# Kernel tuning notes

Measured on AMD Instinct MI355X. Metric: run time of the kernel, lower is better.

Reference implementation:

```python
import jax, jax.numpy as jnp
import numpy as np

B, P, D_IN = 128, 4096, 4   # frames, points/frame, xyz+time
NG = 16                      # number of trajectory groups
H1, H2, H3 = 64, 128, 512    # PointNet shared-MLP widths


def _init_mlp(key, dims):
    ks = jax.random.split(key, len(dims) - 1)
    params = []
    for k, (di, do) in zip(ks, zip(dims[:-1], dims[1:])):
        W = jax.random.normal(k, (di, do), dtype=jnp.float32) * (1.0 / np.sqrt(di))
        b = jnp.zeros((do,), dtype=jnp.float32)
        params.append((W, b))
    return params


def setup_inputs() -> dict:
    key = jax.random.key(0)
    k_pc, k_t, k_idx, k_g, k_l = jax.random.split(key, 5)
    pc = jax.random.normal(k_pc, (B, 3, P), dtype=jnp.float32)
    traj_time_batch = jax.random.uniform(k_t, (B, 1), dtype=jnp.float32)
    traj_inbatch_index = jnp.sort(jax.random.randint(k_idx, (B,), 0, NG)).astype(jnp.int32)
    (Wg1, bg1), (Wg2, bg2), (Wg3, bg3) = _init_mlp(k_g, [D_IN, H1, H2, H3])
    (Wl1, bl1), (Wl2, bl2), (Wl3, bl3) = _init_mlp(k_l, [D_IN, H1, H2, H3])
    return dict(pc=pc, traj_time_batch=traj_time_batch, traj_inbatch_index=traj_inbatch_index,
                Wg1=Wg1, bg1=bg1, Wg2=Wg2, bg2=bg2, Wg3=Wg3, bg3=bg3,
                Wl1=Wl1, bl1=bl1, Wl2=Wl2, bl2=bl2, Wl3=Wl3, bl3=bl3)


def _mlp(x, layers):
    # pointwise shared MLP: x [..., P, d_in] -> [..., P, d_out]
    for W, b in layers:
        x = jax.nn.relu(x @ W + b)
    return x


def reference(pc, traj_time_batch, traj_inbatch_index,
              Wg1, bg1, Wg2, bg2, Wg3, bg3,
              Wl1, bl1, Wl2, bl2, Wl3, bl3):
    b, _, p = pc.shape
    # append time channel: [B,3,P] + [B,1,P] -> [B,4,P]
    t = jnp.broadcast_to(traj_time_batch[..., None], (b, 1, p))
    feat = jnp.concatenate([pc, t], axis=1)
    x = jnp.swapaxes(feat, 1, 2)  # [B,P,4] points-last layout for pointwise MLP

    # global branch: shared MLP on every point, then max over all points of each trajectory group
    hg = _mlp(x, [(Wg1, bg1), (Wg2, bg2), (Wg3, bg3)])           # [B,P,H3]
    seg = jnp.repeat(traj_inbatch_index, p)                       # [B*P]
    gmax = jax.ops.segment_max(hg.reshape(b * p, -1), seg, num_segments=NG)  # [NG,H3]
    global_feat = gmax[traj_inbatch_index]                        # [B,H3] broadcast back per frame

    # local branch: per-frame PointNet encode (shared MLP + max over points)
    hl = _mlp(x, [(Wl1, bl1), (Wl2, bl2), (Wl3, bl3)])            # [B,P,H3]
    local_feat = hl.max(axis=1)                                   # [B,H3]

    z = jnp.concatenate([global_feat, local_feat], axis=1)        # [B,2*H3]
    input_features_vis = pc                                       # original pc (last dim == 4096, no slice)
    return (z, input_features_vis)
```

## Files before the change

kernel.cpp:

```cpp
#include <hip/hip_runtime.h>
#include <hip/hip_bf16.h>

#define NB   128
#define NP   4096
#define NGRP 16
#define C3   512

typedef __bf16 bf16x8 __attribute__((ext_vector_type(8)));
typedef __bf16 bf16x4 __attribute__((ext_vector_type(4)));
typedef float  f32x4  __attribute__((ext_vector_type(4)));

#define WS_W1F_G 0
#define WS_W1F_L 4096
#define WS_W2F_G 8192
#define WS_W2F_L 24576
#define WS_W3F_G 40960
#define WS_W3F_L 172032
#define WS_GMAX  303104

__global__ __launch_bounds__(256) void prep_kernel(
    const float* __restrict__ Wg1, const float* __restrict__ Wg2, const float* __restrict__ Wg3,
    const float* __restrict__ Wl1, const float* __restrict__ Wl2, const float* __restrict__ Wl3,
    const float* __restrict__ pc, float* __restrict__ out, char* __restrict__ ws) {
    const int t = blockIdx.x, tid = threadIdx.x;
    if (t >= 37) {
        const f32x4* src = (const f32x4*)pc;
        f32x4* dst = (f32x4*)(out + NB * 2 * C3);
        int base = (t - 37) * 1024 + tid;
        #pragma unroll
        for (int j = 0; j < 4; ++j) dst[base + j * 256] = src[base + j * 256];
        return;
    }
    if (t == 36) {
        float* gmax = (float*)(ws + WS_GMAX);
        #pragma unroll
        for (int k = 0; k < 32; ++k) gmax[k * 256 + tid] = 0.0f;
        int c = tid >> 6, lane = tid & 63;
        int ch = c * 16 + (lane & 15);
        int kb = (lane >> 4) * 8;
        bf16x8 pg, pl;
        #pragma unroll
        for (int j = 0; j < 8; ++j) {
            int k = kb + j;
            pg[j] = (k < 4) ? (__bf16)Wg1[k * 64 + ch] : (__bf16)0.0f;
            pl[j] = (k < 4) ? (__bf16)Wl1[k * 64 + ch] : (__bf16)0.0f;
        }
        *(bf16x8*)((__bf16*)(ws + WS_W1F_G) + c * 512 + lane * 8) = pg;
        *(bf16x8*)((__bf16*)(ws + WS_W1F_L) + c * 512 + lane * 8) = pl;
        return;
    }
    __shared__ float tile[64][65];
    const float* src; __bf16* dst; int cBase, mMul, srcStride;
    if (t < 32) {
        int branch = t >> 4, rem = t & 15;
        int tk = rem >> 3, tc = rem & 7;
        src = (branch ? Wl3 : Wg3) + (size_t)(tk * 64) * 512 + tc * 64;
        dst = (__bf16*)(ws + (branch ? WS_W3F_L : WS_W3F_G));
        cBase = tc * 16 + tk * 2; mMul = 4; srcStride = 512;
    } else {
        int u = t - 32; int branch = u >> 1, tc = u & 1;
        src = (branch ? Wl2 : Wg2) + tc * 64;
        dst = (__bf16*)(ws + (branch ? WS_W2F_L : WS_W2F_G));
        cBase = tc * 8; mMul = 2; srcStride = 128;
    }
    {
        int r0 = tid >> 6, cl = tid & 63;
        #pragma unroll
        for (int p = 0; p < 16; ++p)
            tile[p * 4 + r0][cl] = src[(size_t)(p * 4 + r0) * srcStride + cl];
    }
    __syncthreads();
    int lane = tid & 63, l15 = lane & 15, q = lane >> 4;
    #pragma unroll
    for (int cc = 0; cc < 2; ++cc) {
        int pair = (tid >> 6) * 2 + cc;
        int mi = pair >> 1, ks = pair & 1;
        bf16x8 pk;
        #pragma unroll
        for (int j = 0; j < 8; ++j) pk[j] = (__bf16)tile[ks * 32 + q * 8 + j][mi * 16 + l15];
        *(bf16x8*)(dst + (cBase + mi * mMul + ks) * 512 + lane * 8) = pk;
    }
}

__global__ __launch_bounds__(512, 2) void main_kernel(
    const float* __restrict__ pc, const float* __restrict__ tt, const int* __restrict__ idx,
    const float* __restrict__ bg1, const float* __restrict__ bg2, const float* __restrict__ bg3,
    const float* __restrict__ bl1, const float* __restrict__ bl2, const float* __restrict__ bl3,
    float* __restrict__ out, char* __restrict__ ws) {
    __shared__ __align__(16) char smem[102912];
    __bf16* h2f = (__bf16*)smem;
    __bf16* w2f = (__bf16*)(smem + 65536);
    __bf16* h1s = (__bf16*)(smem + 81920);
    float*  b2s = (float*)(smem + 102400);

    const int tid = threadIdx.x, lane = tid & 63, wave = tid >> 6;
    const int quad = lane >> 4, l15 = lane & 15;
    const int branch = blockIdx.y, frame = blockIdx.x;

    const __bf16* w1g = (const __bf16*)(ws + (branch ? WS_W1F_L : WS_W1F_G));
    const __bf16* w2g = (const __bf16*)(ws + (branch ? WS_W2F_L : WS_W2F_G));
    const __bf16* w3g = (const __bf16*)(ws + (branch ? WS_W3F_L : WS_W3F_G));
    const float* b1 = branch ? bl1 : bg1;
    const float* b2 = branch ? bl2 : bg2;
    const float* b3 = branch ? bl3 : bg3;

    for (int i = tid; i < 1024; i += 512) ((f32x4*)w2f)[i] = ((const f32x4*)w2g)[i];
    if (tid < 128) b2s[tid] = b2[tid];

    bf16x8 a1[4];
    #pragma unroll
    for (int mi = 0; mi < 4; ++mi) a1[mi] = *(const bf16x8*)(w1g + mi * 512 + lane * 8);
    bf16x8 aw[4][4];
    #pragma unroll
    for (int mi = 0; mi < 4; ++mi)
        #pragma unroll
        for (int ks = 0; ks < 4; ++ks)
            aw[mi][ks] = *(const bf16x8*)(w3g + (wave * 16 + mi * 4 + ks) * 512 + lane * 8);

    float b1r[4][4];
    #pragma unroll
    for (int mi = 0; mi < 4; ++mi)
        #pragma unroll
        for (int r = 0; r < 4; ++r) b1r[mi][r] = b1[mi * 16 + quad * 4 + r];

    const float tval = tt[frame];
    const f32x4 zf = {0.0f, 0.0f, 0.0f, 0.0f};
    f32x4 runmax[4];
    #pragma unroll
    for (int mi = 0; mi < 4; ++mi) runmax[mi] = (f32x4){-1e30f, -1e30f, -1e30f, -1e30f};

    const float* pcx = pc + (size_t)frame * 3 * NP;
    __bf16* hs = h1s + wave * 1280;
    const int pw = wave * 16 + l15;

    float xx = pcx[pw], xy = pcx[NP + pw], xz = pcx[2 * NP + pw];

    __syncthreads();

    {
        bf16x8 xb;
        #pragma unroll
        for (int j = 0; j < 8; ++j) xb[j] = (__bf16)0.0f;
        if (quad == 0) { xb[0] = (__bf16)xx; xb[1] = (__bf16)xy; xb[2] = (__bf16)xz; xb[3] = (__bf16)tval; }
        #pragma unroll
        for (int mi = 0; mi < 4; ++mi) {
            f32x4 c = __builtin_amdgcn_mfma_f32_16x16x32_bf16(a1[mi], xb, zf, 0, 0, 0);
            bf16x4 pk;
            #pragma unroll
            for (int r = 0; r < 4; ++r) pk[r] = (__bf16)fmaxf(c[r] + b1r[mi][r], 0.0f);
            *(bf16x4*)(hs + l15 * 80 + mi * 16 + quad * 4) = pk;
        }
        bf16x8 hbf0 = *(const bf16x8*)(hs + l15 * 80 + quad * 8);
        bf16x8 hbf1 = *(const bf16x8*)(hs + l15 * 80 + 32 + quad * 8);
        #pragma unroll
        for (int mi = 0; mi < 8; ++mi) {
            bf16x8 a20 = *(const bf16x8*)(w2f + (mi * 2) * 512 + lane * 8);
            bf16x8 a21 = *(const bf16x8*)(w2f + (mi * 2 + 1) * 512 + lane * 8);
            f32x4 c = __builtin_amdgcn_mfma_f32_16x16x32_bf16(a20, hbf0, zf, 0, 0, 0);
            c = __builtin_amdgcn_mfma_f32_16x16x32_bf16(a21, hbf1, c, 0, 0, 0);
            f32x4 bb = *(const f32x4*)(b2s + mi * 16 + quad * 4);
            bf16x4 pk;
            #pragma unroll
            for (int r = 0; r < 4; ++r) pk[r] = (__bf16)fmaxf(c[r] + bb[r], 0.0f);
            const int c0 = mi * 16 + quad * 4;
            *(bf16x4*)(h2f + ((wave * 4 + (c0 >> 5)) * 4 + ((c0 >> 3) & 3)) * 128 + l15 * 8 + (c0 & 7)) = pk;
        }
    }

    for (int m = 0; m < 32; ++m) {
        __syncthreads();
        const __bf16* hb = h2f + (m & 1) * 16384;
        __bf16* hbn = h2f + ((m + 1) & 1) * 16384;
        const bool more = (m < 31);
        float nx = 0.f, ny = 0.f, nz = 0.f;
        if (more) {
            const int p = (m + 1) * 128 + pw;
            nx = pcx[p]; ny = pcx[NP + p]; nz = pcx[2 * NP + p];
        }
        bf16x8 hbf0, hbf1;
        bf16x8 bh0[4], bh1[4];
        #pragma unroll
        for (int ks = 0; ks < 4; ++ks) bh0[ks] = *(const bf16x8*)(hb + ks * 512 + lane * 8);
        #pragma unroll
        for (int ni = 0; ni < 8; ++ni) {
            bf16x8* cur = (ni & 1) ? bh1 : bh0;
            bf16x8* nxt = (ni & 1) ? bh0 : bh1;
            if (ni < 7) {
                #pragma unroll
                for (int ks = 0; ks < 4; ++ks)
                    nxt[ks] = *(const bf16x8*)(hb + ((ni + 1) * 4 + ks) * 512 + lane * 8);
            }
            f32x4 acc[4];
            #pragma unroll
            for (int ks = 0; ks < 4; ++ks)
                #pragma unroll
                for (int mi = 0; mi < 4; ++mi)
                    acc[mi] = __builtin_amdgcn_mfma_f32_16x16x32_bf16(
                        aw[mi][ks], cur[ks], ks ? acc[mi] : zf, 0, 0, 0);
            #pragma unroll
            for (int mi = 0; mi < 4; ++mi)
                #pragma unroll
                for (int r = 0; r < 4; ++r)
                    runmax[mi][r] = fmaxf(runmax[mi][r], acc[mi][r]);

            if (more && ni == 2) {
                bf16x8 xb;
                #pragma unroll
                for (int j = 0; j < 8; ++j) xb[j] = (__bf16)0.0f;
                if (quad == 0) { xb[0] = (__bf16)nx; xb[1] = (__bf16)ny; xb[2] = (__bf16)nz; xb[3] = (__bf16)tval; }
                #pragma unroll
                for (int mi = 0; mi < 4; ++mi) {
                    f32x4 c = __builtin_amdgcn_mfma_f32_16x16x32_bf16(a1[mi], xb, zf, 0, 0, 0);
                    bf16x4 pk;
                    #pragma unroll
                    for (int r = 0; r < 4; ++r) pk[r] = (__bf16)fmaxf(c[r] + b1r[mi][r], 0.0f);
                    *(bf16x4*)(hs + l15 * 80 + mi * 16 + quad * 4) = pk;
                }
            }
            if (more && ni == 4) {
                hbf0 = *(const bf16x8*)(hs + l15 * 80 + quad * 8);
                hbf1 = *(const bf16x8*)(hs + l15 * 80 + 32 + quad * 8);
            }
            if (more && ni == 6) {
                #pragma unroll
                for (int mi = 0; mi < 8; ++mi) {
                    bf16x8 a20 = *(const bf16x8*)(w2f + (mi * 2) * 512 + lane * 8);
                    bf16x8 a21 = *(const bf16x8*)(w2f + (mi * 2 + 1) * 512 + lane * 8);
                    f32x4 c = __builtin_amdgcn_mfma_f32_16x16x32_bf16(a20, hbf0, zf, 0, 0, 0);
                    c = __builtin_amdgcn_mfma_f32_16x16x32_bf16(a21, hbf1, c, 0, 0, 0);
                    f32x4 bb = *(const f32x4*)(b2s + mi * 16 + quad * 4);
                    bf16x4 pk;
                    #pragma unroll
                    for (int r = 0; r < 4; ++r) pk[r] = (__bf16)fmaxf(c[r] + bb[r], 0.0f);
                    const int c0 = mi * 16 + quad * 4;
                    *(bf16x4*)(hbn + ((wave * 4 + (c0 >> 5)) * 4 + ((c0 >> 3) & 3)) * 128 + l15 * 8 + (c0 & 7)) = pk;
                }
            }
        }
    }

    const int g = idx[frame];
    float* gmax = (float*)(ws + WS_GMAX);
    #pragma unroll
    for (int mi = 0; mi < 4; ++mi) {
        f32x4 v = runmax[mi];
        #pragma unroll
        for (int d = 1; d < 16; d <<= 1) {
            #pragma unroll
            for (int r = 0; r < 4; ++r) v[r] = fmaxf(v[r], __shfl_xor(v[r], d));
        }
        if (l15 == 0) {
            #pragma unroll
            for (int r = 0; r < 4; ++r) {
                const int ch = wave * 64 + mi * 16 + quad * 4 + r;
                const float fv = fmaxf(v[r] + b3[ch], 0.0f);
                if (branch == 0)
                    atomicMax((unsigned*)(gmax + g * C3 + ch), __float_as_uint(fv));
                else
                    out[(size_t)frame * (2 * C3) + C3 + ch] = fv;
            }
        }
    }
}

__global__ void gather_kernel(const int* __restrict__ idx, const char* __restrict__ ws,
                              float* __restrict__ out) {
    int i = blockIdx.x * blockDim.x + threadIdx.x;
    int b = i >> 9, ch = i & 511;
    const float* gmax = (const float*)(ws + WS_GMAX);
    out[b * (2 * C3) + ch] = gmax[idx[b] * C3 + ch];
}

extern "C" void kernel_launch(void* const* d_in, const int* in_sizes, int n_in,
                              void* d_out, int out_size, void* d_ws, size_t ws_size,
                              hipStream_t stream) {
    const float* pc  = (const float*)d_in[0];
    const float* tt  = (const float*)d_in[1];
    const int*   idx = (const int*)d_in[2];
    const float* Wg1 = (const float*)d_in[3];  const float* bg1 = (const float*)d_in[4];
    const float* Wg2 = (const float*)d_in[5];  const float* bg2 = (const float*)d_in[6];
    const float* Wg3 = (const float*)d_in[7];  const float* bg3 = (const float*)d_in[8];
    const float* Wl1 = (const float*)d_in[9];  const float* bl1 = (const float*)d_in[10];
    const float* Wl2 = (const float*)d_in[11]; const float* bl2 = (const float*)d_in[12];
    const float* Wl3 = (const float*)d_in[13]; const float* bl3 = (const float*)d_in[14];
    float* out = (float*)d_out;
    char*  ws  = (char*)d_ws;

    prep_kernel<<<421, 256, 0, stream>>>(Wg1, Wg2, Wg3, Wl1, Wl2, Wl3, pc, out, ws);
    main_kernel<<<dim3(128, 2), 512, 0, stream>>>(pc, tt, idx, bg1, bg2, bg3,
                                                  bl1, bl2, bl3, out, ws);
    gather_kernel<<<256, 256, 0, stream>>>(idx, ws, out);
}
```

Measured before the change: 202.2 us.

## Split layer-3 channels across wave slices and compute layer-2 cooperatively per block

Reorganizes main_kernel so each wave holds a 128-channel slice of W3 (8x4 fragments) covering half the points, and layers 1 and 2 are computed cooperatively with W2 fragments held in registers instead of LDS. Per-wave maxima are combined through shared memory before the bias, ReLU and atomic or store. The pc passthrough copy moves from prep_kernel into main_kernel's branch-0 blocks, shrinking the prep launch. This trades more register pressure (32 W3 fragments per wave) and extra barriers for better operand reuse and less LDS traffic and footprint.

```diff
diff --git a/kernel.cpp b/kernel.cpp
--- a/kernel.cpp
+++ b/kernel.cpp
@@ -21,16 +21,8 @@
 __global__ __launch_bounds__(256) void prep_kernel(
     const float* __restrict__ Wg1, const float* __restrict__ Wg2, const float* __restrict__ Wg3,
     const float* __restrict__ Wl1, const float* __restrict__ Wl2, const float* __restrict__ Wl3,
-    const float* __restrict__ pc, float* __restrict__ out, char* __restrict__ ws) {
+    char* __restrict__ ws) {
     const int t = blockIdx.x, tid = threadIdx.x;
-    if (t >= 37) {
-        const f32x4* src = (const f32x4*)pc;
-        f32x4* dst = (f32x4*)(out + NB * 2 * C3);
-        int base = (t - 37) * 1024 + tid;
-        #pragma unroll
-        for (int j = 0; j < 4; ++j) dst[base + j * 256] = src[base + j * 256];
-        return;
-    }
     if (t == 36) {
         float* gmax = (float*)(ws + WS_GMAX);
         #pragma unroll
@@ -87,15 +79,24 @@
     const float* __restrict__ bg1, const float* __restrict__ bg2, const float* __restrict__ bg3,
     const float* __restrict__ bl1, const float* __restrict__ bl2, const float* __restrict__ bl3,
     float* __restrict__ out, char* __restrict__ ws) {
-    __shared__ __align__(16) char smem[102912];
+    __shared__ __align__(16) char smem[82688];
     __bf16* h2f = (__bf16*)smem;
-    __bf16* w2f = (__bf16*)(smem + 65536);
-    __bf16* h1s = (__bf16*)(smem + 81920);
-    float*  b2s = (float*)(smem + 102400);
+    __bf16* h1f = (__bf16*)(smem + 65536);
+    float*  b1s = (float*)(smem + 81920);
+    float*  b2s = (float*)(smem + 82176);
 
     const int tid = threadIdx.x, lane = tid & 63, wave = tid >> 6;
     const int quad = lane >> 4, l15 = lane & 15;
     const int branch = blockIdx.y, frame = blockIdx.x;
+    const int half = wave >> 2;
+    const int slice = wave & 3;
+
+    if (branch == 0) {
+        const f32x4* ps = (const f32x4*)(pc + (size_t)frame * 3 * NP);
+        f32x4* pd = (f32x4*)(out + NB * 2 * C3 + (size_t)frame * 3 * NP);
+        #pragma unroll
+        for (int j = 0; j < 6; ++j) pd[j * 512 + tid] = ps[j * 512 + tid];
+    }
 
     const __bf16* w1g = (const __bf16*)(ws + (branch ? WS_W1F_L : WS_W1F_G));
     const __bf16* w2g = (const __bf16*)(ws + (branch ? WS_W2F_L : WS_W2F_G));
@@ -104,40 +105,35 @@
     const float* b2 = branch ? bl2 : bg2;
     const float* b3 = branch ? bl3 : bg3;
 
-    for (int i = tid; i < 1024; i += 512) ((f32x4*)w2f)[i] = ((const f32x4*)w2g)[i];
+    if (tid < 64)  b1s[tid] = b1[tid];
     if (tid < 128) b2s[tid] = b2[tid];
 
     bf16x8 a1[4];
     #pragma unroll
     for (int mi = 0; mi < 4; ++mi) a1[mi] = *(const bf16x8*)(w1g + mi * 512 + lane * 8);
-    bf16x8 aw[4][4];
-    #pragma unroll
-    for (int mi = 0; mi < 4; ++mi)
+    bf16x8 a2[2][2];
+    #pragma unroll
+    for (int mi = 0; mi < 2; ++mi)
+        #pragma unroll
+        for (int ks = 0; ks < 2; ++ks)
+            a2[mi][ks] = *(const bf16x8*)(w2g + ((slice * 2 + mi) * 2 + ks) * 512 + lane * 8);
+    bf16x8 aw[8][4];
+    #pragma unroll
+    for (int mi = 0; mi < 8; ++mi)
         #pragma unroll
         for (int ks = 0; ks < 4; ++ks)
-            aw[mi][ks] = *(const bf16x8*)(w3g + (wave * 16 + mi * 4 + ks) * 512 + lane * 8);
-
-    float b1r[4][4];
-    #pragma unroll
-    for (int mi = 0; mi < 4; ++mi)
-        #pragma unroll
-        for (int r = 0; r < 4; ++r) b1r[mi][r] = b1[mi * 16 + quad * 4 + r];
+            aw[mi][ks] = *(const bf16x8*)(w3g + ((slice * 8 + mi) * 4 + ks) * 512 + lane * 8);
 
     const float tval = tt[frame];
     const f32x4 zf = {0.0f, 0.0f, 0.0f, 0.0f};
-    f32x4 runmax[4];
-    #pragma unroll
-    for (int mi = 0; mi < 4; ++mi) runmax[mi] = (f32x4){-1e30f, -1e30f, -1e30f, -1e30f};
+    f32x4 runmax[8];
+    #pragma unroll
+    for (int mi = 0; mi < 8; ++mi) runmax[mi] = (f32x4){-1e30f, -1e30f, -1e30f, -1e30f};
 
     const float* pcx = pc + (size_t)frame * 3 * NP;
-    __bf16* hs = h1s + wave * 1280;
     const int pw = wave * 16 + l15;
 
-    float xx = pcx[pw], xy = pcx[NP + pw], xz = pcx[2 * NP + pw];
-
-    __syncthreads();
-
-    {
+    auto do_l1 = [&](float xx, float xy, float xz) {
         bf16x8 xb;
         #pragma unroll
         for (int j = 0; j < 8; ++j) xb[j] = (__bf16)0.0f;
@@ -145,26 +141,63 @@
         #pragma unroll
         for (int mi = 0; mi < 4; ++mi) {
             f32x4 c = __builtin_amdgcn_mfma_f32_16x16x32_bf16(a1[mi], xb, zf, 0, 0, 0);
+            f32x4 bv = *(const f32x4*)(b1s + mi * 16 + quad * 4);
             bf16x4 pk;
             #pragma unroll
-            for (int r = 0; r < 4; ++r) pk[r] = (__bf16)fmaxf(c[r] + b1r[mi][r], 0.0f);
-            *(bf16x4*)(hs + l15 * 80 + mi * 16 + quad * 4) = pk;
-        }
-        bf16x8 hbf0 = *(const bf16x8*)(hs + l15 * 80 + quad * 8);
-        bf16x8 hbf1 = *(const bf16x8*)(hs + l15 * 80 + 32 + quad * 8);
-        #pragma unroll
-        for (int mi = 0; mi < 8; ++mi) {
-            bf16x8 a20 = *(const bf16x8*)(w2f + (mi * 2) * 512 + lane * 8);
-            bf16x8 a21 = *(const bf16x8*)(w2f + (mi * 2 + 1) * 512 + lane * 8);
-            f32x4 c = __builtin_amdgcn_mfma_f32_16x16x32_bf16(a20, hbf0, zf, 0, 0, 0);
-            c = __builtin_amdgcn_mfma_f32_16x16x32_bf16(a21, hbf1, c, 0, 0, 0);
-            f32x4 bb = *(const f32x4*)(b2s + mi * 16 + quad * 4);
-            bf16x4 pk;
-            #pragma unroll
-            for (int r = 0; r < 4; ++r) pk[r] = (__bf16)fmaxf(c[r] + bb[r], 0.0f);
-            const int c0 = mi * 16 + quad * 4;
-            *(bf16x4*)(h2f + ((wave * 4 + (c0 >> 5)) * 4 + ((c0 >> 3) & 3)) * 128 + l15 * 8 + (c0 & 7)) = pk;
-        }
+            for (int r = 0; r < 4; ++r) pk[r] = (__bf16)fmaxf(c[r] + bv[r], 0.0f);
+            const int kq = (mi & 1) * 2 + (quad >> 1);
+            *(bf16x4*)(h1f + (wave * 2 + (mi >> 1)) * 512 + kq * 128 + l15 * 8 + (quad & 1) * 4) = pk;
+        }
+    };
+    auto do_l2 = [&](__bf16* hbn) {
+        #pragma unroll
+        for (int ni = 0; ni < 4; ++ni) {
+            const int p16 = half * 4 + ni;
+            bf16x8 q0 = *(const bf16x8*)(h1f + (p16 * 2 + 0) * 512 + lane * 8);
+            bf16x8 q1 = *(const bf16x8*)(h1f + (p16 * 2 + 1) * 512 + lane * 8);
+            #pragma unroll
+            for (int mi = 0; mi < 2; ++mi) {
+                f32x4 c = __builtin_amdgcn_mfma_f32_16x16x32_bf16(a2[mi][0], q0, zf, 0, 0, 0);
+                c = __builtin_amdgcn_mfma_f32_16x16x32_bf16(a2[mi][1], q1, c, 0, 0, 0);
+                f32x4 bv = *(const f32x4*)(b2s + slice * 32 + mi * 16 + quad * 4);
+                bf16x4 pk;
+                #pragma unroll
+                for (int r = 0; r < 4; ++r) pk[r] = (__bf16)fmaxf(c[r] + bv[r], 0.0f);
+                const int kq = mi * 2 + (quad >> 1);
+                *(bf16x4*)(hbn + (p16 * 4 + slice) * 512 + kq * 128 + l15 * 8 + (quad & 1) * 4) = pk;
+            }
+        }
+    };
+    auto p2_pair = [&](const __bf16* hb, int p16base) {
+        bf16x8 bhA[4], bhB[4];
+        #pragma unroll
+        for (int ks = 0; ks < 4; ++ks)
+            bhA[ks] = *(const bf16x8*)(hb + (p16base * 4 + ks) * 512 + lane * 8);
+        #pragma unroll
+        for (int ks = 0; ks < 4; ++ks)
+            bhB[ks] = *(const bf16x8*)(hb + ((p16base + 1) * 4 + ks) * 512 + lane * 8);
+        #pragma unroll
+        for (int u = 0; u < 2; ++u) {
+            const bf16x8* cur = u ? bhB : bhA;
+            #pragma unroll
+            for (int mi = 0; mi < 8; ++mi) {
+                f32x4 acc = __builtin_amdgcn_mfma_f32_16x16x32_bf16(aw[mi][0], cur[0], zf, 0, 0, 0);
+                acc = __builtin_amdgcn_mfma_f32_16x16x32_bf16(aw[mi][1], cur[1], acc, 0, 0, 0);
+                acc = __builtin_amdgcn_mfma_f32_16x16x32_bf16(aw[mi][2], cur[2], acc, 0, 0, 0);
+                acc = __builtin_amdgcn_mfma_f32_16x16x32_bf16(aw[mi][3], cur[3], acc, 0, 0, 0);
+                #pragma unroll
+                for (int r = 0; r < 4; ++r) runmax[mi][r] = fmaxf(runmax[mi][r], acc[r]);
+            }
+        }
+    };
+
+    __syncthreads();
+
+    {
+        float xx = pcx[pw], xy = pcx[NP + pw], xz = pcx[2 * NP + pw];
+        do_l1(xx, xy, xz);
+        __syncthreads();
+        do_l2(h2f);
     }
 
     for (int m = 0; m < 32; ++m) {
@@ -177,72 +210,17 @@
             const int p = (m + 1) * 128 + pw;
             nx = pcx[p]; ny = pcx[NP + p]; nz = pcx[2 * NP + p];
         }
-        bf16x8 hbf0, hbf1;
-        bf16x8 bh0[4], bh1[4];
-        #pragma unroll
-        for (int ks = 0; ks < 4; ++ks) bh0[ks] = *(const bf16x8*)(hb + ks * 512 + lane * 8);
-        #pragma unroll
-        for (int ni = 0; ni < 8; ++ni) {
-            bf16x8* cur = (ni & 1) ? bh1 : bh0;
-            bf16x8* nxt = (ni & 1) ? bh0 : bh1;
-            if (ni < 7) {
-                #pragma unroll
-                for (int ks = 0; ks < 4; ++ks)
-                    nxt[ks] = *(const bf16x8*)(hb + ((ni + 1) * 4 + ks) * 512 + lane * 8);
-            }
-            f32x4 acc[4];
-            #pragma unroll
-            for (int ks = 0; ks < 4; ++ks)
-                #pragma unroll
-                for (int mi = 0; mi < 4; ++mi)
-                    acc[mi] = __builtin_amdgcn_mfma_f32_16x16x32_bf16(
-                        aw[mi][ks], cur[ks], ks ? acc[mi] : zf, 0, 0, 0);
-            #pragma unroll
-            for (int mi = 0; mi < 4; ++mi)
-                #pragma unroll
-                for (int r = 0; r < 4; ++r)
-                    runmax[mi][r] = fmaxf(runmax[mi][r], acc[mi][r]);
-
-            if (more && ni == 2) {
-                bf16x8 xb;
-                #pragma unroll
-                for (int j = 0; j < 8; ++j) xb[j] = (__bf16)0.0f;
-                if (quad == 0) { xb[0] = (__bf16)nx; xb[1] = (__bf16)ny; xb[2] = (__bf16)nz; xb[3] = (__bf16)tval; }
-                #pragma unroll
-                for (int mi = 0; mi < 4; ++mi) {
-                    f32x4 c = __builtin_amdgcn_mfma_f32_16x16x32_bf16(a1[mi], xb, zf, 0, 0, 0);
-                    bf16x4 pk;
-                    #pragma unroll
-                    for (int r = 0; r < 4; ++r) pk[r] = (__bf16)fmaxf(c[r] + b1r[mi][r], 0.0f);
-                    *(bf16x4*)(hs + l15 * 80 + mi * 16 + quad * 4) = pk;
-                }
-            }
-            if (more && ni == 4) {
-                hbf0 = *(const bf16x8*)(hs + l15 * 80 + quad * 8);
-                hbf1 = *(const bf16x8*)(hs + l15 * 80 + 32 + quad * 8);
-            }
-            if (more && ni == 6) {
-                #pragma unroll
-                for (int mi = 0; mi < 8; ++mi) {
-                    bf16x8 a20 = *(const bf16x8*)(w2f + (mi * 2) * 512 + lane * 8);
-                    bf16x8 a21 = *(const bf16x8*)(w2f + (mi * 2 + 1) * 512 + lane * 8);
-                    f32x4 c = __builtin_amdgcn_mfma_f32_16x16x32_bf16(a20, hbf0, zf, 0, 0, 0);
-                    c = __builtin_amdgcn_mfma_f32_16x16x32_bf16(a21, hbf1, c, 0, 0, 0);
-                    f32x4 bb = *(const f32x4*)(b2s + mi * 16 + quad * 4);
-                    bf16x4 pk;
-                    #pragma unroll
-                    for (int r = 0; r < 4; ++r) pk[r] = (__bf16)fmaxf(c[r] + bb[r], 0.0f);
-                    const int c0 = mi * 16 + quad * 4;
-                    *(bf16x4*)(hbn + ((wave * 4 + (c0 >> 5)) * 4 + ((c0 >> 3) & 3)) * 128 + l15 * 8 + (c0 & 7)) = pk;
-                }
-            }
-        }
-    }
-
-    const int g = idx[frame];
-    float* gmax = (float*)(ws + WS_GMAX);
-    #pragma unroll
-    for (int mi = 0; mi < 4; ++mi) {
+        p2_pair(hb, half * 4 + 0);
+        if (more) do_l1(nx, ny, nz);
+        __syncthreads();
+        p2_pair(hb, half * 4 + 2);
+        if (more) do_l2(hbn);
+    }
+
+    __syncthreads();
+    float* fscr = (float*)h1f;
+    #pragma unroll
+    for (int mi = 0; mi < 8; ++mi) {
         f32x4 v = runmax[mi];
         #pragma unroll
         for (int d = 1; d < 16; d <<= 1) {
@@ -251,15 +229,20 @@
         }
         if (l15 == 0) {
             #pragma unroll
-            for (int r = 0; r < 4; ++r) {
-                const int ch = wave * 64 + mi * 16 + quad * 4 + r;
-                const float fv = fmaxf(v[r] + b3[ch], 0.0f);
-                if (branch == 0)
-                    atomicMax((unsigned*)(gmax + g * C3 + ch), __float_as_uint(fv));
-                else
-                    out[(size_t)frame * (2 * C3) + C3 + ch] = fv;
-            }
-        }
+            for (int r = 0; r < 4; ++r)
+                fscr[half * 512 + slice * 128 + mi * 16 + quad * 4 + r] = v[r];
+        }
+    }
+    __syncthreads();
+    {
+        const int g = idx[frame];
+        float* gmax = (float*)(ws + WS_GMAX);
+        float v = fmaxf(fscr[tid], fscr[512 + tid]);
+        v = fmaxf(v + b3[tid], 0.0f);
+        if (branch == 0)
+            atomicMax((unsigned*)(gmax + g * C3 + tid), __float_as_uint(v));
+        else
+            out[(size_t)frame * (2 * C3) + C3 + tid] = v;
     }
 }
 
@@ -286,7 +269,7 @@
     float* out = (float*)d_out;
     char*  ws  = (char*)d_ws;
 
-    prep_kernel<<<421, 256, 0, stream>>>(Wg1, Wg2, Wg3, Wl1, Wl2, Wl3, pc, out, ws);
+    prep_kernel<<<37, 256, 0, stream>>>(Wg1, Wg2, Wg3, Wl1, Wl2, Wl3, ws);
     main_kernel<<<dim3(128, 2), 512, 0, stream>>>(pc, tt, idx, bg1, bg2, bg3,
                                                   bl1, bl2, bl3, out, ws);
     gather_kernel<<<256, 256, 0, stream>>>(idx, ws, out);
```

Result: slower. 242.8 us (+20.1%).
